# Optimization experiments

Measured on AMD Instinct MI355X. Metric: run time of the kernel, lower is better.

Reference implementation:

```python
import jax, jax.numpy as jnp
import numpy as np

B, S, E, H = 4, 2048, 1024, 16
D = E // H  # head_size = 64

def setup_inputs() -> dict:
    key = jax.random.key(0)
    k1, k2, k3 = jax.random.split(key, 3)
    x = jax.random.normal(k1, (B, S, E), dtype=jnp.float32)
    # torch Linear weight is (out,in); we store transposed (in,out) for x @ W
    w_attn = jax.random.normal(k2, (E, 3 * E), dtype=jnp.float32) * (1.0 / np.sqrt(E))
    w_proj = jax.random.normal(k3, (E, E), dtype=jnp.float32) * (1.0 / np.sqrt(E))
    return {"x": x, "w_attn": w_attn, "w_proj": w_proj}

def reference(x, w_attn, w_proj):
    b, s, e = x.shape
    qkv = x @ w_attn                      # (B,S,3E)
    q, k, v = jnp.split(qkv, 3, axis=2)
    # (B,S,H,D) -> (B,H,S,D)
    q = q.reshape(b, s, H, D).transpose(0, 2, 1, 3)
    k = k.reshape(b, s, H, D).transpose(0, 2, 1, 3)
    v = v.reshape(b, s, H, D).transpose(0, 2, 1, 3)
    scale = 1.0 / np.sqrt(D).astype(np.float32)
    att = jnp.einsum('bhqd,bhkd->bhqk', q, k) * scale  # (B,H,S,S)
    causal = jnp.tril(jnp.ones((s, s), dtype=bool))
    att = jnp.where(causal[None, None, :, :], att, jnp.float32(-jnp.inf))
    att = jax.nn.softmax(att, axis=-1)
    # dropout layers are identity in eval mode
    y = jnp.einsum('bhqk,bhkd->bhqd', att, v)          # (B,H,S,D)
    y = y.transpose(0, 2, 1, 3).reshape(b, s, e)       # (B,S,E)
    return y @ w_proj
```

## Files before the change

kernel.cpp:

```cpp
#include <hip/hip_runtime.h>
#include <hip/hip_bf16.h>
#include <cstdint>

typedef __attribute__((ext_vector_type(8))) short bf16x8;
typedef __attribute__((ext_vector_type(4))) short short4v;
typedef __attribute__((ext_vector_type(4))) float f32x4;

#define MFMA(a, b, c) __builtin_amdgcn_mfma_f32_16x16x32_bf16((a), (b), (c), 0, 0, 0)

__device__ __forceinline__ unsigned short f2bf(float f) {
  union { float f; unsigned int u; } v;
  v.f = f;
  unsigned int r = v.u + 0x7FFFu + ((v.u >> 16) & 1u);
  return (unsigned short)(r >> 16);
}

__device__ __forceinline__ unsigned short f2bf_ru(float f) {
  union { float f; unsigned int u; } v;
  v.f = f;
  return (unsigned short)((v.u + 0x8000u) >> 16);
}

__device__ __forceinline__ void async_cp16(const unsigned short* g, unsigned short* l) {
  __builtin_amdgcn_global_load_lds(
      (const __attribute__((address_space(1))) unsigned int*)g,
      (__attribute__((address_space(3))) unsigned int*)l, 16, 0, 0);
}

__global__ __launch_bounds__(256) void cvt_x(const float* __restrict__ in,
                                             unsigned short* __restrict__ out) {
  size_t i = ((size_t)blockIdx.x * 256 + threadIdx.x) * 8;
  float4 a = *(const float4*)(in + i);
  float4 b = *(const float4*)(in + i + 4);
  bf16x8 p;
  p[0] = (short)f2bf(a.x); p[1] = (short)f2bf(a.y);
  p[2] = (short)f2bf(a.z); p[3] = (short)f2bf(a.w);
  p[4] = (short)f2bf(b.x); p[5] = (short)f2bf(b.y);
  p[6] = (short)f2bf(b.z); p[7] = (short)f2bf(b.w);
  *(bf16x8*)(out + i) = p;
}

__global__ __launch_bounds__(256) void transpose_cvt(const float* __restrict__ in,
                                                     unsigned short* __restrict__ out,
                                                     int K, int N) {
  __shared__ float tile[64][65];
  int k0 = blockIdx.x * 64;
  int n0 = blockIdx.y * 64;
  int c = threadIdx.x & 63;
  int rb = threadIdx.x >> 6;
#pragma unroll
  for (int i = 0; i < 16; ++i) {
    int r = rb * 16 + i;
    tile[r][c] = in[(size_t)(k0 + r) * N + (n0 + c)];
  }
  __syncthreads();
#pragma unroll
  for (int i = 0; i < 16; ++i) {
    int r = rb * 16 + i;
    out[(size_t)(n0 + r) * K + (k0 + c)] = f2bf(tile[c][r]);
  }
}

__global__ __launch_bounds__(256) void gemm_qkv(const unsigned short* __restrict__ X,
                                                const unsigned short* __restrict__ WT,
                                                unsigned short* __restrict__ qb,
                                                unsigned short* __restrict__ kb,
                                                unsigned short* __restrict__ vt) {
  const int K = 1024;
  __shared__ unsigned short As[128 * 32];
  __shared__ unsigned short Bs[128 * 32];
  int t = threadIdx.x, lane = t & 63, w = t >> 6;
  int quad = lane >> 4, l15 = lane & 15;
  int wm = (w >> 1) * 64, wn = (w & 1) * 64;
  int row0 = blockIdx.y * 128, col0 = blockIdx.x * 128;
  int srow = w * 32 + (lane >> 2);
  int scol = (lane & 3) * 8;
  const unsigned short* a0 = X + (size_t)(row0 + srow) * K + scol;
  const unsigned short* a1 = X + (size_t)(row0 + srow + 16) * K + scol;
  const unsigned short* b0 = WT + (size_t)(col0 + srow) * K + scol;
  const unsigned short* b1 = WT + (size_t)(col0 + srow + 16) * K + scol;
  unsigned short* lA0 = &As[w * 1024];
  unsigned short* lA1 = &As[w * 1024 + 512];
  unsigned short* lB0 = &Bs[w * 1024];
  unsigned short* lB1 = &Bs[w * 1024 + 512];
  f32x4 zero4 = {0.f, 0.f, 0.f, 0.f};
  f32x4 acc[4][4];
#pragma unroll
  for (int i = 0; i < 4; ++i)
#pragma unroll
    for (int j = 0; j < 4; ++j) acc[i][j] = zero4;

  for (int k0 = 0; k0 < K; k0 += 32) {
    __syncthreads();
    async_cp16(a0 + k0, lA0);
    async_cp16(a1 + k0, lA1);
    async_cp16(b0 + k0, lB0);
    async_cp16(b1 + k0, lB1);
    __syncthreads();
    bf16x8 af[4], bfr[4];
#pragma unroll
    for (int mt = 0; mt < 4; ++mt)
      af[mt] = *(const bf16x8*)&As[(wm + mt * 16 + l15) * 32 + quad * 8];
#pragma unroll
    for (int nt = 0; nt < 4; ++nt)
      bfr[nt] = *(const bf16x8*)&Bs[(wn + nt * 16 + l15) * 32 + quad * 8];
#pragma unroll
    for (int mt = 0; mt < 4; ++mt)
#pragma unroll
      for (int nt = 0; nt < 4; ++nt)
        acc[mt][nt] = MFMA(af[mt], bfr[nt], acc[mt][nt]);
  }

  const float qscale = 0.125f * 1.4426950408889634f;
#pragma unroll
  for (int mt = 0; mt < 4; ++mt) {
    int rix0 = row0 + wm + mt * 16 + quad * 4;
    int b = rix0 >> 11;
    int s0 = rix0 & 2047;
#pragma unroll
    for (int nt = 0; nt < 4; ++nt) {
      int c = col0 + wn + nt * 16 + l15;
      int which = c >> 10;
      int e = c & 1023;
      int h = e >> 6, d = e & 63;
      size_t bh = (size_t)b * 16 + h;
      if (which == 2) {
        short4v pv;
#pragma unroll
        for (int r = 0; r < 4; ++r) pv[r] = (short)f2bf(acc[mt][nt][r]);
        *(short4v*)(vt + (bh * 64 + d) * 2048 + s0) = pv;
      } else {
        unsigned short* dst = (which == 0) ? qb : kb;
        float sc = (which == 0) ? qscale : 1.0f;
#pragma unroll
        for (int r = 0; r < 4; ++r)
          dst[(bh * 2048 + (s0 + r)) * 64 + d] = f2bf(acc[mt][nt][r] * sc);
      }
    }
  }
}

__global__ __launch_bounds__(256) void flash_attn(const unsigned short* __restrict__ qb,
                                                  const unsigned short* __restrict__ kb,
                                                  const unsigned short* __restrict__ vt,
                                                  unsigned short* __restrict__ yb) {
  __shared__ unsigned short Ks[64 * 68];
  __shared__ unsigned short Vs[64 * 68];
  __shared__ unsigned short P[4][16 * 68];
  int idx = blockIdx.x;
  int qt = 15 - (idx >> 6);
  int bh = idx & 63;
  int t = threadIdx.x, lane = t & 63, w = t >> 6;
  int quad = lane >> 4, l15 = lane & 15;
  int qrow0 = qt * 128 + w * 32;

  bf16x8 aq0[2], aq1[2];
#pragma unroll
  for (int s = 0; s < 2; ++s) {
    const unsigned short* Qp =
        qb + ((size_t)bh * 2048 + qrow0 + s * 16 + l15) * 64 + quad * 8;
    aq0[s] = *(const bf16x8*)Qp;
    aq1[s] = *(const bf16x8*)(Qp + 32);
  }
  f32x4 zero4 = {0.f, 0.f, 0.f, 0.f};
  f32x4 o[2][4], accl[2];
#pragma unroll
  for (int s = 0; s < 2; ++s) {
    accl[s] = zero4;
#pragma unroll
    for (int nt = 0; nt < 4; ++nt) o[s][nt] = zero4;
  }
  bf16x8 ones;
#pragma unroll
  for (int i = 0; i < 8; ++i) ones[i] = (short)0x3F80;
  unsigned short* Pw = P[w];

  int srow = t >> 2;
  int sseg = (t & 3) * 8;
  const unsigned short* Kg = kb + ((size_t)bh * 2048 + srow) * 64 + sseg;
  const unsigned short* Vg = vt + ((size_t)bh * 64 + srow) * 2048 + sseg;
  int ktmax = 2 * qt + 1;

  bf16x8 kg0 = *(const bf16x8*)Kg;
  bf16x8 kg1 = *(const bf16x8*)(Kg + 32);
  bf16x8 vg0 = *(const bf16x8*)Vg;
  bf16x8 vg1 = *(const bf16x8*)(Vg + 32);

  for (int kt = 0; kt <= ktmax; ++kt) {
    int kbase = kt * 64;
    __syncthreads();
    *(bf16x8*)&Ks[srow * 68 + sseg] = kg0;
    *(bf16x8*)&Ks[srow * 68 + sseg + 32] = kg1;
    *(bf16x8*)&Vs[srow * 68 + sseg] = vg0;
    *(bf16x8*)&Vs[srow * 68 + sseg + 32] = vg1;
    __syncthreads();
    if (kt < ktmax) {
      const unsigned short* nk = Kg + (size_t)(kbase + 64) * 64;
      kg0 = *(const bf16x8*)nk;
      kg1 = *(const bf16x8*)(nk + 32);
      const unsigned short* nv = Vg + kbase + 64;
      vg0 = *(const bf16x8*)nv;
      vg1 = *(const bf16x8*)(nv + 32);
    }
    if (kbase > qrow0 + 31) continue;

    bf16x8 kf0[4], kf1[4], vf0[4], vf1[4];
#pragma unroll
    for (int nt = 0; nt < 4; ++nt) {
      kf0[nt] = *(const bf16x8*)&Ks[(nt * 16 + l15) * 68 + quad * 8];
      kf1[nt] = *(const bf16x8*)&Ks[(nt * 16 + l15) * 68 + 32 + quad * 8];
      vf0[nt] = *(const bf16x8*)&Vs[(nt * 16 + l15) * 68 + quad * 8];
      vf1[nt] = *(const bf16x8*)&Vs[(nt * 16 + l15) * 68 + 32 + quad * 8];
    }

#pragma unroll
    for (int s = 0; s < 2; ++s) {
      int rowb = qrow0 + s * 16;
      if (kbase > rowb + 15) continue;
      f32x4 sv[4];
#pragma unroll
      for (int nt = 0; nt < 4; ++nt) {
        f32x4 z = zero4;
        z = MFMA(aq0[s], kf0[nt], z);
        z = MFMA(aq1[s], kf1[nt], z);
        sv[nt] = z;
      }
      if (kbase + 63 > rowb) {
#pragma unroll
        for (int nt = 0; nt < 4; ++nt) {
          int col = kbase + nt * 16 + l15;
#pragma unroll
          for (int r = 0; r < 4; ++r)
            if (col > rowb + quad * 4 + r) sv[nt][r] = -1e30f;
        }
      }
#pragma unroll
      for (int nt = 0; nt < 4; ++nt)
#pragma unroll
        for (int r = 0; r < 4; ++r) {
          float p = __builtin_amdgcn_exp2f(sv[nt][r]);
          Pw[(quad * 4 + r) * 68 + nt * 16 + l15] = f2bf_ru(p);
        }
      bf16x8 ap0 = *(const bf16x8*)&Pw[l15 * 68 + quad * 8];
      bf16x8 ap1 = *(const bf16x8*)&Pw[l15 * 68 + 32 + quad * 8];
      accl[s] = MFMA(ap0, ones, accl[s]);
      accl[s] = MFMA(ap1, ones, accl[s]);
#pragma unroll
      for (int nt = 0; nt < 4; ++nt) {
        o[s][nt] = MFMA(ap0, vf0[nt], o[s][nt]);
        o[s][nt] = MFMA(ap1, vf1[nt], o[s][nt]);
      }
    }
  }

  int b = bh >> 4, h = bh & 15;
#pragma unroll
  for (int s = 0; s < 2; ++s) {
    float inv[4];
#pragma unroll
    for (int r = 0; r < 4; ++r) inv[r] = 1.0f / accl[s][r];
#pragma unroll
    for (int nt = 0; nt < 4; ++nt) {
      int e = h * 64 + nt * 16 + l15;
#pragma unroll
      for (int r = 0; r < 4; ++r) {
        int srow_g = qrow0 + s * 16 + quad * 4 + r;
        yb[((size_t)b * 2048 + srow_g) * 1024 + e] = f2bf(o[s][nt][r] * inv[r]);
      }
    }
  }
}

__global__ __launch_bounds__(256) void gemm_proj(const unsigned short* __restrict__ Y,
                                                 const unsigned short* __restrict__ WT,
                                                 float* __restrict__ out) {
  const int K = 1024;
  __shared__ unsigned short As[128 * 32];
  __shared__ unsigned short Bs[128 * 32];
  int t = threadIdx.x, lane = t & 63, w = t >> 6;
  int quad = lane >> 4, l15 = lane & 15;
  int wm = (w >> 1) * 64, wn = (w & 1) * 64;
  int row0 = blockIdx.y * 128, col0 = blockIdx.x * 128;
  int srow = w * 32 + (lane >> 2);
  int scol = (lane & 3) * 8;
  const unsigned short* a0 = Y + (size_t)(row0 + srow) * K + scol;
  const unsigned short* a1 = Y + (size_t)(row0 + srow + 16) * K + scol;
  const unsigned short* b0 = WT + (size_t)(col0 + srow) * K + scol;
  const unsigned short* b1 = WT + (size_t)(col0 + srow + 16) * K + scol;
  unsigned short* lA0 = &As[w * 1024];
  unsigned short* lA1 = &As[w * 1024 + 512];
  unsigned short* lB0 = &Bs[w * 1024];
  unsigned short* lB1 = &Bs[w * 1024 + 512];
  f32x4 zero4 = {0.f, 0.f, 0.f, 0.f};
  f32x4 acc[4][4];
#pragma unroll
  for (int i = 0; i < 4; ++i)
#pragma unroll
    for (int j = 0; j < 4; ++j) acc[i][j] = zero4;

  for (int k0 = 0; k0 < K; k0 += 32) {
    __syncthreads();
    async_cp16(a0 + k0, lA0);
    async_cp16(a1 + k0, lA1);
    async_cp16(b0 + k0, lB0);
    async_cp16(b1 + k0, lB1);
    __syncthreads();
    bf16x8 af[4], bfr[4];
#pragma unroll
    for (int mt = 0; mt < 4; ++mt)
      af[mt] = *(const bf16x8*)&As[(wm + mt * 16 + l15) * 32 + quad * 8];
#pragma unroll
    for (int nt = 0; nt < 4; ++nt)
      bfr[nt] = *(const bf16x8*)&Bs[(wn + nt * 16 + l15) * 32 + quad * 8];
#pragma unroll
    for (int mt = 0; mt < 4; ++mt)
#pragma unroll
      for (int nt = 0; nt < 4; ++nt)
        acc[mt][nt] = MFMA(af[mt], bfr[nt], acc[mt][nt]);
  }

#pragma unroll
  for (int mt = 0; mt < 4; ++mt) {
    int rix0 = row0 + wm + mt * 16 + quad * 4;
#pragma unroll
    for (int nt = 0; nt < 4; ++nt) {
      int c = col0 + wn + nt * 16 + l15;
#pragma unroll
      for (int r = 0; r < 4; ++r)
        out[(size_t)(rix0 + r) * 1024 + c] = acc[mt][nt][r];
    }
  }
}

extern "C" void kernel_launch(void* const* d_in, const int* in_sizes, int n_in,
                              void* d_out, int out_size, void* d_ws, size_t ws_size,
                              hipStream_t stream) {
  const float* x = (const float*)d_in[0];
  const float* w_attn = (const float*)d_in[1];
  const float* w_proj = (const float*)d_in[2];
  float* out = (float*)d_out;
  char* ws = (char*)d_ws;
  unsigned short* wT  = (unsigned short*)(ws + 0);
  unsigned short* wpT = (unsigned short*)(ws + 6291456);
  unsigned short* qb  = (unsigned short*)(ws + 8388608);
  unsigned short* kb  = (unsigned short*)(ws + 25165824);
  unsigned short* vt  = (unsigned short*)(ws + 41943040);
  unsigned short* xyb = (unsigned short*)(ws + 58720256);

  cvt_x<<<4096, 256, 0, stream>>>(x, xyb);
  transpose_cvt<<<dim3(16, 48), 256, 0, stream>>>(w_attn, wT, 1024, 3072);
  transpose_cvt<<<dim3(16, 16), 256, 0, stream>>>(w_proj, wpT, 1024, 1024);
  gemm_qkv<<<dim3(24, 64), 256, 0, stream>>>(xyb, wT, qb, kb, vt);
  flash_attn<<<dim3(1024), 256, 0, stream>>>(qb, kb, vt, xyb);
  gemm_proj<<<dim3(8, 64), 256, 0, stream>>>(xyb, wpT, out);
}
```

Measured before the change: 284.9 us.

## Widen GEMM K-tile with XOR-swizzled LDS and shrink attention query tile

Both GEMMs now stage a 64-wide K slice per iteration into XOR-swizzled shared memory. This halves the number of barrier pairs and is meant to avoid LDS bank conflicts on the fragment reads. The flash attention kernel drops from 128 to 64 query rows per block, one 16-row strip per wave, and launches twice as many blocks. That gives finer causal load balance and lower register use, but each loaded K/V tile is now reused by fewer query rows.

Result: no change. 281.3 us (-1.3%).

```diff
diff --git a/kernel.cpp b/kernel.cpp
--- a/kernel.cpp
+++ b/kernel.cpp
@@ -67,22 +67,19 @@
                                                 unsigned short* __restrict__ kb,
                                                 unsigned short* __restrict__ vt) {
   const int K = 1024;
-  __shared__ unsigned short As[128 * 32];
-  __shared__ unsigned short Bs[128 * 32];
+  __shared__ unsigned short As[128 * 64];
+  __shared__ unsigned short Bs[128 * 64];
   int t = threadIdx.x, lane = t & 63, w = t >> 6;
   int quad = lane >> 4, l15 = lane & 15;
+  int sl7 = l15 & 7;
   int wm = (w >> 1) * 64, wn = (w & 1) * 64;
   int row0 = blockIdx.y * 128, col0 = blockIdx.x * 128;
-  int srow = w * 32 + (lane >> 2);
-  int scol = (lane & 3) * 8;
-  const unsigned short* a0 = X + (size_t)(row0 + srow) * K + scol;
-  const unsigned short* a1 = X + (size_t)(row0 + srow + 16) * K + scol;
-  const unsigned short* b0 = WT + (size_t)(col0 + srow) * K + scol;
-  const unsigned short* b1 = WT + (size_t)(col0 + srow + 16) * K + scol;
-  unsigned short* lA0 = &As[w * 1024];
-  unsigned short* lA1 = &As[w * 1024 + 512];
-  unsigned short* lB0 = &Bs[w * 1024];
-  unsigned short* lB1 = &Bs[w * 1024 + 512];
+  int srow = w * 8 + (lane >> 3);
+  int schunk = (lane & 7) ^ (lane >> 3);
+  const unsigned short* aSrc = X + (size_t)(row0 + srow) * K + schunk * 8;
+  const unsigned short* bSrc = WT + (size_t)(col0 + srow) * K + schunk * 8;
+  unsigned short* ldsA = &As[(w * 8) * 64];
+  unsigned short* ldsB = &Bs[(w * 8) * 64];
   f32x4 zero4 = {0.f, 0.f, 0.f, 0.f};
   f32x4 acc[4][4];
 #pragma unroll
@@ -90,25 +87,32 @@
 #pragma unroll
     for (int j = 0; j < 4; ++j) acc[i][j] = zero4;
 
-  for (int k0 = 0; k0 < K; k0 += 32) {
-    __syncthreads();
-    async_cp16(a0 + k0, lA0);
-    async_cp16(a1 + k0, lA1);
-    async_cp16(b0 + k0, lB0);
-    async_cp16(b1 + k0, lB1);
-    __syncthreads();
-    bf16x8 af[4], bfr[4];
-#pragma unroll
-    for (int mt = 0; mt < 4; ++mt)
-      af[mt] = *(const bf16x8*)&As[(wm + mt * 16 + l15) * 32 + quad * 8];
-#pragma unroll
-    for (int nt = 0; nt < 4; ++nt)
-      bfr[nt] = *(const bf16x8*)&Bs[(wn + nt * 16 + l15) * 32 + quad * 8];
-#pragma unroll
-    for (int mt = 0; mt < 4; ++mt)
+  for (int k0 = 0; k0 < K; k0 += 64) {
+    __syncthreads();
+#pragma unroll
+    for (int i = 0; i < 4; ++i)
+      async_cp16(aSrc + (size_t)i * 32 * K + k0, ldsA + i * 32 * 64);
+#pragma unroll
+    for (int i = 0; i < 4; ++i)
+      async_cp16(bSrc + (size_t)i * 32 * K + k0, ldsB + i * 32 * 64);
+    __syncthreads();
+#pragma unroll
+    for (int h = 0; h < 2; ++h) {
+      bf16x8 af[4], bfr[4];
+#pragma unroll
+      for (int mt = 0; mt < 4; ++mt)
+        af[mt] = *(const bf16x8*)&As[(wm + mt * 16 + l15) * 64 +
+                                     ((h * 4 + quad) ^ sl7) * 8];
 #pragma unroll
       for (int nt = 0; nt < 4; ++nt)
-        acc[mt][nt] = MFMA(af[mt], bfr[nt], acc[mt][nt]);
+        bfr[nt] = *(const bf16x8*)&Bs[(wn + nt * 16 + l15) * 64 +
+                                      ((h * 4 + quad) ^ sl7) * 8];
+#pragma unroll
+      for (int mt = 0; mt < 4; ++mt)
+#pragma unroll
+        for (int nt = 0; nt < 4; ++nt)
+          acc[mt][nt] = MFMA(af[mt], bfr[nt], acc[mt][nt]);
+    }
   }
 
   const float qscale = 0.125f * 1.4426950408889634f;
@@ -148,28 +152,20 @@
   __shared__ unsigned short Vs[64 * 68];
   __shared__ unsigned short P[4][16 * 68];
   int idx = blockIdx.x;
-  int qt = 15 - (idx >> 6);
+  int qt = 31 - (idx >> 6);
   int bh = idx & 63;
   int t = threadIdx.x, lane = t & 63, w = t >> 6;
   int quad = lane >> 4, l15 = lane & 15;
-  int qrow0 = qt * 128 + w * 32;
-
-  bf16x8 aq0[2], aq1[2];
-#pragma unroll
-  for (int s = 0; s < 2; ++s) {
-    const unsigned short* Qp =
-        qb + ((size_t)bh * 2048 + qrow0 + s * 16 + l15) * 64 + quad * 8;
-    aq0[s] = *(const bf16x8*)Qp;
-    aq1[s] = *(const bf16x8*)(Qp + 32);
-  }
+  int qrow0 = qt * 64 + w * 16;
+
+  const unsigned short* Qp = qb + ((size_t)bh * 2048 + qrow0 + l15) * 64 + quad * 8;
+  bf16x8 aq0 = *(const bf16x8*)Qp;
+  bf16x8 aq1 = *(const bf16x8*)(Qp + 32);
   f32x4 zero4 = {0.f, 0.f, 0.f, 0.f};
-  f32x4 o[2][4], accl[2];
-#pragma unroll
-  for (int s = 0; s < 2; ++s) {
-    accl[s] = zero4;
-#pragma unroll
-    for (int nt = 0; nt < 4; ++nt) o[s][nt] = zero4;
-  }
+  f32x4 o[4], accl;
+  accl = zero4;
+#pragma unroll
+  for (int nt = 0; nt < 4; ++nt) o[nt] = zero4;
   bf16x8 ones;
 #pragma unroll
   for (int i = 0; i < 8; ++i) ones[i] = (short)0x3F80;
@@ -179,7 +175,7 @@
   int sseg = (t & 3) * 8;
   const unsigned short* Kg = kb + ((size_t)bh * 2048 + srow) * 64 + sseg;
   const unsigned short* Vg = vt + ((size_t)bh * 64 + srow) * 2048 + sseg;
-  int ktmax = 2 * qt + 1;
+  int ktmax = qt;
 
   bf16x8 kg0 = *(const bf16x8*)Kg;
   bf16x8 kg1 = *(const bf16x8*)(Kg + 32);
@@ -202,7 +198,7 @@
       vg0 = *(const bf16x8*)nv;
       vg1 = *(const bf16x8*)(nv + 32);
     }
-    if (kbase > qrow0 + 31) continue;
+    if (kbase > qrow0 + 15) continue;
 
     bf16x8 kf0[4], kf1[4], vf0[4], vf1[4];
 #pragma unroll
@@ -213,60 +209,52 @@
       vf1[nt] = *(const bf16x8*)&Vs[(nt * 16 + l15) * 68 + 32 + quad * 8];
     }
 
-#pragma unroll
-    for (int s = 0; s < 2; ++s) {
-      int rowb = qrow0 + s * 16;
-      if (kbase > rowb + 15) continue;
-      f32x4 sv[4];
+    f32x4 sv[4];
+#pragma unroll
+    for (int nt = 0; nt < 4; ++nt) {
+      f32x4 z = zero4;
+      z = MFMA(aq0, kf0[nt], z);
+      z = MFMA(aq1, kf1[nt], z);
+      sv[nt] = z;
+    }
+    if (kbase + 63 > qrow0) {
 #pragma unroll
       for (int nt = 0; nt < 4; ++nt) {
-        f32x4 z = zero4;
-        z = MFMA(aq0[s], kf0[nt], z);
-        z = MFMA(aq1[s], kf1[nt], z);
-        sv[nt] = z;
+        int col = kbase + nt * 16 + l15;
+#pragma unroll
+        for (int r = 0; r < 4; ++r)
+          if (col > qrow0 + quad * 4 + r) sv[nt][r] = -1e30f;
       }
-      if (kbase + 63 > rowb) {
-#pragma unroll
-        for (int nt = 0; nt < 4; ++nt) {
-          int col = kbase + nt * 16 + l15;
-#pragma unroll
-          for (int r = 0; r < 4; ++r)
-            if (col > rowb + quad * 4 + r) sv[nt][r] = -1e30f;
-        }
+    }
+#pragma unroll
+    for (int nt = 0; nt < 4; ++nt)
+#pragma unroll
+      for (int r = 0; r < 4; ++r) {
+        float p = __builtin_amdgcn_exp2f(sv[nt][r]);
+        Pw[(quad * 4 + r) * 68 + nt * 16 + l15] = f2bf_ru(p);
       }
-#pragma unroll
-      for (int nt = 0; nt < 4; ++nt)
-#pragma unroll
-        for (int r = 0; r < 4; ++r) {
-          float p = __builtin_amdgcn_exp2f(sv[nt][r]);
-          Pw[(quad * 4 + r) * 68 + nt * 16 + l15] = f2bf_ru(p);
-        }
-      bf16x8 ap0 = *(const bf16x8*)&Pw[l15 * 68 + quad * 8];
-      bf16x8 ap1 = *(const bf16x8*)&Pw[l15 * 68 + 32 + quad * 8];
-      accl[s] = MFMA(ap0, ones, accl[s]);
-      accl[s] = MFMA(ap1, ones, accl[s]);
-#pragma unroll
-      for (int nt = 0; nt < 4; ++nt) {
-        o[s][nt] = MFMA(ap0, vf0[nt], o[s][nt]);
-        o[s][nt] = MFMA(ap1, vf1[nt], o[s][nt]);
-      }
+    bf16x8 ap0 = *(const bf16x8*)&Pw[l15 * 68 + quad * 8];
+    bf16x8 ap1 = *(const bf16x8*)&Pw[l15 * 68 + 32 + quad * 8];
+    accl = MFMA(ap0, ones, accl);
+    accl = MFMA(ap1, ones, accl);
+#pragma unroll
+    for (int nt = 0; nt < 4; ++nt) {
+      o[nt] = MFMA(ap0, vf0[nt], o[nt]);
+      o[nt] = MFMA(ap1, vf1[nt], o[nt]);
     }
   }
 
   int b = bh >> 4, h = bh & 15;
-#pragma unroll
-  for (int s = 0; s < 2; ++s) {
-    float inv[4];
-#pragma unroll
-    for (int r = 0; r < 4; ++r) inv[r] = 1.0f / accl[s][r];
-#pragma unroll
-    for (int nt = 0; nt < 4; ++nt) {
-      int e = h * 64 + nt * 16 + l15;
-#pragma unroll
-      for (int r = 0; r < 4; ++r) {
-        int srow_g = qrow0 + s * 16 + quad * 4 + r;
-        yb[((size_t)b * 2048 + srow_g) * 1024 + e] = f2bf(o[s][nt][r] * inv[r]);
-      }
+  float inv[4];
+#pragma unroll
+  for (int r = 0; r < 4; ++r) inv[r] = 1.0f / accl[r];
+#pragma unroll
+  for (int nt = 0; nt < 4; ++nt) {
+    int e = h * 64 + nt * 16 + l15;
+#pragma unroll
+    for (int r = 0; r < 4; ++r) {
+      int srow_g = qrow0 + quad * 4 + r;
+      yb[((size_t)b * 2048 + srow_g) * 1024 + e] = f2bf(o[nt][r] * inv[r]);
     }
   }
 }
@@ -275,22 +263,19 @@
                                                  const unsigned short* __restrict__ WT,
                                                  float* __restrict__ out) {
   const int K = 1024;
-  __shared__ unsigned short As[128 * 32];
-  __shared__ unsigned short Bs[128 * 32];
+  __shared__ unsigned short As[128 * 64];
+  __shared__ unsigned short Bs[128 * 64];
   int t = threadIdx.x, lane = t & 63, w = t >> 6;
   int quad = lane >> 4, l15 = lane & 15;
+  int sl7 = l15 & 7;
   int wm = (w >> 1) * 64, wn = (w & 1) * 64;
   int row0 = blockIdx.y * 128, col0 = blockIdx.x * 128;
-  int srow = w * 32 + (lane >> 2);
-  int scol = (lane & 3) * 8;
-  const unsigned short* a0 = Y + (size_t)(row0 + srow) * K + scol;
-  const unsigned short* a1 = Y + (size_t)(row0 + srow + 16) * K + scol;
-  const unsigned short* b0 = WT + (size_t)(col0 + srow) * K + scol;
-  const unsigned short* b1 = WT + (size_t)(col0 + srow + 16) * K + scol;
-  unsigned short* lA0 = &As[w * 1024];
-  unsigned short* lA1 = &As[w * 1024 + 512];
-  unsigned short* lB0 = &Bs[w * 1024];
-  unsigned short* lB1 = &Bs[w * 1024 + 512];
+  int srow = w * 8 + (lane >> 3);
+  int schunk = (lane & 7) ^ (lane >> 3);
+  const unsigned short* aSrc = Y + (size_t)(row0 + srow) * K + schunk * 8;
+  const unsigned short* bSrc = WT + (size_t)(col0 + srow) * K + schunk * 8;
+  unsigned short* ldsA = &As[(w * 8) * 64];
+  unsigned short* ldsB = &Bs[(w * 8) * 64];
   f32x4 zero4 = {0.f, 0.f, 0.f, 0.f};
   f32x4 acc[4][4];
 #pragma unroll
@@ -298,25 +283,32 @@
 #pragma unroll
     for (int j = 0; j < 4; ++j) acc[i][j] = zero4;
 
-  for (int k0 = 0; k0 < K; k0 += 32) {
-    __syncthreads();
-    async_cp16(a0 + k0, lA0);
-    async_cp16(a1 + k0, lA1);
-    async_cp16(b0 + k0, lB0);
-    async_cp16(b1 + k0, lB1);
-    __syncthreads();
-    bf16x8 af[4], bfr[4];
-#pragma unroll
-    for (int mt = 0; mt < 4; ++mt)
-      af[mt] = *(const bf16x8*)&As[(wm + mt * 16 + l15) * 32 + quad * 8];
-#pragma unroll
-    for (int nt = 0; nt < 4; ++nt)
-      bfr[nt] = *(const bf16x8*)&Bs[(wn + nt * 16 + l15) * 32 + quad * 8];
-#pragma unroll
-    for (int mt = 0; mt < 4; ++mt)
+  for (int k0 = 0; k0 < K; k0 += 64) {
+    __syncthreads();
+#pragma unroll
+    for (int i = 0; i < 4; ++i)
+      async_cp16(aSrc + (size_t)i * 32 * K + k0, ldsA + i * 32 * 64);
+#pragma unroll
+    for (int i = 0; i < 4; ++i)
+      async_cp16(bSrc + (size_t)i * 32 * K + k0, ldsB + i * 32 * 64);
+    __syncthreads();
+#pragma unroll
+    for (int h = 0; h < 2; ++h) {
+      bf16x8 af[4], bfr[4];
+#pragma unroll
+      for (int mt = 0; mt < 4; ++mt)
+        af[mt] = *(const bf16x8*)&As[(wm + mt * 16 + l15) * 64 +
+                                     ((h * 4 + quad) ^ sl7) * 8];
 #pragma unroll
       for (int nt = 0; nt < 4; ++nt)
-        acc[mt][nt] = MFMA(af[mt], bfr[nt], acc[mt][nt]);
+        bfr[nt] = *(const bf16x8*)&Bs[(wn + nt * 16 + l15) * 64 +
+                                      ((h * 4 + quad) ^ sl7) * 8];
+#pragma unroll
+      for (int mt = 0; mt < 4; ++mt)
+#pragma unroll
+        for (int nt = 0; nt < 4; ++nt)
+          acc[mt][nt] = MFMA(af[mt], bfr[nt], acc[mt][nt]);
+    }
   }
 
 #pragma unroll
@@ -351,6 +343,6 @@
   transpose_cvt<<<dim3(16, 48), 256, 0, stream>>>(w_attn, wT, 1024, 3072);
   transpose_cvt<<<dim3(16, 16), 256, 0, stream>>>(w_proj, wpT, 1024, 1024);
   gemm_qkv<<<dim3(24, 64), 256, 0, stream>>>(xyb, wT, qb, kb, vt);
-  flash_attn<<<dim3(1024), 256, 0, stream>>>(qb, kb, vt, xyb);
+  flash_attn<<<dim3(2048), 256, 0, stream>>>(qb, kb, vt, xyb);
   gemm_proj<<<dim3(8, 64), 256, 0, stream>>>(xyb, wpT, out);
 }
```
